# Performance work log

Hardware: AMD Instinct MI355X
Metric: run time of the kernel (lower is better)

Reference implementation:

```python
import jax, jax.numpy as jnp
import numpy as np

B, L, D = 4, 4096, 128
BLOCK, SPARSITY = 64, 0.9
NEG = -1e9


def _make_block_mask(key):
    nb = L // BLOCK
    bm = jax.random.uniform(key, (nb, nb)) > SPARSITY
    bm = bm | jnp.eye(nb, dtype=bool)  # keep diagonal blocks so no row is fully masked
    bm = jnp.tril(bm)
    return jnp.repeat(jnp.repeat(bm, BLOCK, axis=0), BLOCK, axis=1)  # [L, L]


def _xavier(key, shape):
    limit = float(np.sqrt(6.0 / (shape[0] + shape[1])))
    return jax.random.uniform(key, shape, jnp.float32, -limit, limit)


def setup_inputs() -> dict:
    key = jax.random.key(0)
    ks = jax.random.split(key, 10)
    t = lambda k: jax.random.normal(k, (B, L, D), jnp.float32)
    return {
        'q_real': t(ks[0]), 'q_imag': t(ks[1]),
        'k_real': t(ks[2]), 'k_imag': t(ks[3]),
        'v_real': t(ks[4]), 'v_imag': t(ks[5]),
        'W_qkv': _xavier(ks[6], (6 * D, 6 * D)),
        'b_qkv': jnp.zeros((6 * D,), jnp.float32),
        'W_out': _xavier(ks[7], (2 * D, 2 * D)),
        'b_out': jnp.zeros((2 * D,), jnp.float32),
        'block_mask': _make_block_mask(ks[8]),
    }


def reference(q_real, q_imag, k_real, k_imag, v_real, v_imag,
              W_qkv, b_qkv, W_out, b_out, block_mask):
    d = q_real.shape[-1]
    scale = d ** -0.5
    # fused qkv projection over the 6 concatenated channels
    x = jnp.concatenate([q_real, q_imag, k_real, k_imag, v_real, v_imag], axis=-1)  # [B,L,6D]
    qkv = (x @ W_qkv.T + b_qkv).reshape(x.shape[0], x.shape[1], 6, d)
    q_r, q_i, k_r, k_i, v_r, v_i = (qkv[:, :, j] for j in range(6))

    def attn(q, k, v):
        s = jnp.einsum('bqd,bkd->bqk', q, k) * scale          # [B,L,L]
        s = jnp.where(block_mask[None], s, NEG)               # block-sparse mask
        a = jax.nn.softmax(s, axis=-1)                        # dropout = identity (eval)
        return jnp.einsum('bqk,bkd->bqd', a, v)

    out = jnp.concatenate([attn(q_r, k_r, v_r), attn(q_i, k_i, v_i)], axis=-1)  # [B,L,2D]
    out = out @ W_out.T + b_out
    return out[..., :d], out[..., d:]
```

## Files before the change

### kernel.cpp

```cpp
#include <hip/hip_runtime.h>
#include <hip/hip_bf16.h>

typedef unsigned short u16;
typedef __attribute__((ext_vector_type(8))) short bf16x8;
typedef __attribute__((ext_vector_type(4))) float f32x4;

#define SEQ_L 4096
#define M_TOT 16384

__device__ __forceinline__ float bf2f(u16 x) {
    unsigned u = ((unsigned)x) << 16;
    return __builtin_bit_cast(float, u);
}
__device__ __forceinline__ u16 f2bf(float f) {
    unsigned u = __builtin_bit_cast(unsigned, f);
    u += 0x7FFFu + ((u >> 16) & 1u);
    return (u16)(u >> 16);
}
__device__ __forceinline__ void gload16(const u16* g, u16* l) {
    __builtin_amdgcn_global_load_lds(
        (const __attribute__((address_space(1))) unsigned int*)g,
        (__attribute__((address_space(3))) unsigned int*)l, 16, 0, 0);
}

__global__ __launch_bounds__(256) void prep_all(
    const float* __restrict__ in0, const float* __restrict__ in1, const float* __restrict__ in2,
    const float* __restrict__ in3, const float* __restrict__ in4, const float* __restrict__ in5,
    const float* __restrict__ Wqkv, const float* __restrict__ Wout, const void* __restrict__ mask,
    u16* __restrict__ x, u16* __restrict__ Wqkv_bf, u16* __restrict__ Wout_bf,
    unsigned long long* __restrict__ bmap) {
    int id = blockIdx.x * 256 + threadIdx.x;
    if (id < 1572864) {
        const float* ins[6] = {in0, in1, in2, in3, in4, in5};
        int which = id >> 18, j = id & 262143;
        int m = j >> 4, c8 = j & 15;
        const float* sp = ins[which] + (size_t)m * 128 + c8 * 8;
        float4 a = *(const float4*)sp;
        float4 b = *(const float4*)(sp + 4);
        u16 t[8] = {f2bf(a.x), f2bf(a.y), f2bf(a.z), f2bf(a.w),
                    f2bf(b.x), f2bf(b.y), f2bf(b.z), f2bf(b.w)};
        *(uint4*)(x + (size_t)m * 768 + which * 128 + c8 * 8) = *(uint4*)t;
    } else if (id < 1572864 + 73728 + 8192) {
        int i = id - 1572864;
        const float* src = (i < 73728) ? Wqkv : Wout;
        u16* dst = (i < 73728) ? Wqkv_bf : Wout_bf;
        if (i >= 73728) i -= 73728;
        const float* sp = src + (size_t)i * 8;
        float4 a = *(const float4*)sp;
        float4 b = *(const float4*)(sp + 4);
        u16 t[8] = {f2bf(a.x), f2bf(a.y), f2bf(a.z), f2bf(a.w),
                    f2bf(b.x), f2bf(b.y), f2bf(b.z), f2bf(b.w)};
        *(uint4*)(dst + (size_t)i * 8) = *(uint4*)t;
    } else if (id < 1572864 + 73728 + 8192 + 4096) {
        int i = id - 1572864 - 73728 - 8192;
        int bi = i >> 6, bj = i & 63;
        size_t e = (size_t)(bi * 64) * SEQ_L + (size_t)bj * 64;
        const unsigned char* p8 = (const unsigned char*)mask;
        unsigned w0 = *(const unsigned*)mask;
        bool v;
        if (w0 == 0x01010101u || w0 == 0xFFFFFFFFu)      v = p8[e] != 0;
        else if (w0 == 0x3F803F80u || w0 == 0x3C003C00u) v = ((const u16*)mask)[e] != 0;
        else                                             v = ((const unsigned*)mask)[e] != 0;
        unsigned long long bits = __ballot(v);
        if ((i & 63) == 0) bmap[bi] = bits;
    }
}

__global__ __launch_bounds__(256, 3) void qkv_gemm(
    const u16* __restrict__ X, const u16* __restrict__ W, const float* __restrict__ bias,
    u16* __restrict__ qk, u16* __restrict__ vt) {
    __shared__ __align__(16) u16 As[128 * 64];
    __shared__ __align__(16) u16 Bs[128 * 64];
    int m0 = blockIdx.x * 128, n0 = blockIdx.y * 128;
    int tid = threadIdx.x, lane = tid & 63, w = tid >> 6;
    int ln = lane & 15, quad = lane >> 4;
    int rw = (w >> 1) * 64, cw = (w & 1) * 64;
    int lr8 = lane >> 3, lc = lane & 7;
    f32x4 acc[4][4] = {};
    for (int kk = 0; kk < 768; kk += 64) {
        __syncthreads();
        #pragma unroll
        for (int j = 0; j < 4; j++) {
            int r0 = w * 32 + j * 8, r = r0 + lr8;
            gload16(X + (size_t)(m0 + r) * 768 + kk + ((lc ^ (r & 7)) * 8), As + r0 * 64 + lane * 8);
            gload16(W + (size_t)(n0 + r) * 768 + kk + ((lc ^ (r & 7)) * 8), Bs + r0 * 64 + lane * 8);
        }
        __syncthreads();
        #pragma unroll
        for (int s = 0; s < 2; s++) {
            bf16x8 af[4], bfr[4];
            #pragma unroll
            for (int i = 0; i < 4; i++) {
                int R = rw + i * 16 + ln;
                af[i] = *(const bf16x8*)(As + R * 64 + ((4 * s + quad) ^ (ln & 7)) * 8);
            }
            #pragma unroll
            for (int t = 0; t < 4; t++) {
                int R = cw + t * 16 + ln;
                bfr[t] = *(const bf16x8*)(Bs + R * 64 + ((4 * s + quad) ^ (ln & 7)) * 8);
            }
            #pragma unroll
            for (int i = 0; i < 4; i++)
                #pragma unroll
                for (int t = 0; t < 4; t++)
                    acc[i][t] = __builtin_amdgcn_mfma_f32_16x16x32_bf16(af[i], bfr[t], acc[i][t], 0, 0, 0);
        }
    }
    if (n0 < 512) {
        #pragma unroll
        for (int i = 0; i < 4; i++) {
            int row0 = m0 + rw + i * 16 + 4 * quad;
            #pragma unroll
            for (int t = 0; t < 4; t++) {
                int col = n0 + cw + t * 16 + ln;
                float bv = bias[col];
                #pragma unroll
                for (int r = 0; r < 4; r++)
                    qk[(size_t)(row0 + r) * 512 + col] = f2bf(acc[i][t][r] + bv);
            }
        }
    } else {
        #pragma unroll
        for (int i = 0; i < 4; i++) {
            int row0 = m0 + rw + i * 16 + 4 * quad;
            int b = row0 >> 12, seq = row0 & 4095;
            #pragma unroll
            for (int t = 0; t < 4; t++) {
                int col = n0 + cw + t * 16 + ln;
                float bv = bias[col];
                int d = col - 512;
                u16 pk[4] = {f2bf(acc[i][t][0] + bv), f2bf(acc[i][t][1] + bv),
                             f2bf(acc[i][t][2] + bv), f2bf(acc[i][t][3] + bv)};
                *(ushort4*)(vt + ((size_t)(b * 2 + (d >> 7)) * 128 + (d & 127)) * SEQ_L + seq)
                    = *(ushort4*)pk;
            }
        }
    }
}

__global__ __launch_bounds__(256, 2) void attn_sparse(
    const u16* __restrict__ qk, const u16* __restrict__ vt,
    const unsigned long long* __restrict__ bmap, u16* __restrict__ attn_bf) {
    __shared__ __align__(16) u16 Ks[2][64 * 128];
    __shared__ __align__(16) u16 Vs[2][128 * 64];
    __shared__ __align__(16) u16 Psm[4][16 * 72];

    int lane = threadIdx.x & 63, w = threadIdx.x >> 6;
    int ln = lane & 15, quad = lane >> 4;
    int u = blockIdx.x >> 3, v = blockIdx.x & 7;
    int qi = (u < 32) ? (63 - u) : (u - 32);
    int b = v >> 1, ch = v & 1;
    int rowbase = b * SEQ_L + qi * 64 + w * 16;
    const float scale = 0.08838834764831845f;
    u16* Ps = Psm[w];

    bf16x8 qf[4];
    {
        const u16* qp = qk + (size_t)(rowbase + ln) * 512 + ch * 128;
        #pragma unroll
        for (int s = 0; s < 4; s++) qf[s] = *(const bf16x8*)(qp + 32 * s + 8 * quad);
    }
    bf16x8 onesb;
    #pragma unroll
    for (int j = 0; j < 8; j++) onesb[j] = (short)0x3F80;

    float m_st[4];
    #pragma unroll
    for (int r = 0; r < 4; r++) m_st[r] = -1e30f;
    f32x4 accO[8] = {};
    f32x4 accL = {};

    const u16* kbase0 = qk + (size_t)b * SEQ_L * 512 + 256 + ch * 128;
    const u16* vbase0 = vt + (size_t)(b * 2 + ch) * 128 * SEQ_L;
    unsigned long long bm = bmap[qi];

    int kb = __ffsll(bm) - 1; bm &= bm - 1;
    {
        const u16* kp = kbase0 + (size_t)(kb * 64) * 512;
        const u16* vp = vbase0 + kb * 64;
        #pragma unroll
        for (int j = 0; j < 4; j++) {
            int kr = w * 16 + j * 4 + (lane >> 4);
            gload16(kp + (size_t)kr * 512 + (((lane & 15) ^ (kr & 7)) * 8),
                    Ks[0] + (w * 16 + j * 4) * 128 + lane * 8);
        }
        #pragma unroll
        for (int j = 0; j < 4; j++) {
            int d = w * 32 + j * 8 + (lane >> 3);
            gload16(vp + (size_t)d * SEQ_L + (((lane & 7) ^ (d & 7)) * 8),
                    Vs[0] + (w * 32 + j * 8) * 64 + lane * 8);
        }
    }

    int bufc = 0;
    while (true) {
        int nkb = -1;
        if (bm) {
            nkb = __ffsll(bm) - 1; bm &= bm - 1;
            const u16* kp = kbase0 + (size_t)(nkb * 64) * 512;
            const u16* vp = vbase0 + nkb * 64;
            u16* Kd = Ks[bufc ^ 1];
            u16* Vd = Vs[bufc ^ 1];
            #pragma unroll
            for (int j = 0; j < 4; j++) {
                int kr = w * 16 + j * 4 + (lane >> 4);
                gload16(kp + (size_t)kr * 512 + (((lane & 15) ^ (kr & 7)) * 8),
                        Kd + (w * 16 + j * 4) * 128 + lane * 8);
            }
            #pragma unroll
            for (int j = 0; j < 4; j++) {
                int d = w * 32 + j * 8 + (lane >> 3);
                gload16(vp + (size_t)d * SEQ_L + (((lane & 7) ^ (d & 7)) * 8),
                        Vd + (w * 32 + j * 8) * 64 + lane * 8);
            }
        }
        if (nkb >= 0) __builtin_amdgcn_s_waitcnt(0x0F78);
        else          __builtin_amdgcn_s_waitcnt(0x0F70);
        __builtin_amdgcn_s_barrier();

        const u16* K = Ks[bufc];
        const u16* V = Vs[bufc];

        f32x4 accS[4] = {};
        #pragma unroll
        for (int s = 0; s < 4; s++)
            #pragma unroll
            for (int t = 0; t < 4; t++) {
                bf16x8 kf = *(const bf16x8*)(K + (t * 16 + ln) * 128 +
                                             (((4 * s + quad) ^ (ln & 7)) * 8));
                accS[t] = __builtin_amdgcn_mfma_f32_16x16x32_bf16(qf[s], kf, accS[t], 0, 0, 0);
            }

        float mx[4];
        #pragma unroll
        for (int r = 0; r < 4; r++)
            mx[r] = fmaxf(fmaxf(accS[0][r], accS[1][r]),
                          fmaxf(accS[2][r], accS[3][r])) * scale;
        #pragma unroll
        for (int off = 1; off < 16; off <<= 1) {
            float t0 = __shfl_xor(mx[0], off, 64);
            float t1 = __shfl_xor(mx[1], off, 64);
            float t2 = __shfl_xor(mx[2], off, 64);
            float t3 = __shfl_xor(mx[3], off, 64);
            mx[0] = fmaxf(mx[0], t0); mx[1] = fmaxf(mx[1], t1);
            mx[2] = fmaxf(mx[2], t2); mx[3] = fmaxf(mx[3], t3);
        }
        float alpha[4];
        #pragma unroll
        for (int r = 0; r < 4; r++) {
            float nm = fmaxf(m_st[r], mx[r]);
            alpha[r] = __expf(m_st[r] - nm);
            m_st[r] = nm;
        }
        #pragma unroll
        for (int r = 0; r < 4; r++)
            #pragma unroll
            for (int t = 0; t < 4; t++)
                Ps[(4 * quad + r) * 72 + t * 16 + ln] =
                    f2bf(__expf(accS[t][r] * scale - m_st[r]));
        #pragma unroll
        for (int nt = 0; nt < 8; nt++)
            #pragma unroll
            for (int r = 0; r < 4; r++) accO[nt][r] *= alpha[r];
        #pragma unroll
        for (int r = 0; r < 4; r++) accL[r] *= alpha[r];

        #pragma unroll
        for (int h = 0; h < 2; h++) {
            bf16x8 pf = *(const bf16x8*)(Ps + ln * 72 + h * 32 + 8 * quad);
            accL = __builtin_amdgcn_mfma_f32_16x16x32_bf16(pf, onesb, accL, 0, 0, 0);
            #pragma unroll
            for (int nt = 0; nt < 8; nt++) {
                bf16x8 vf = *(const bf16x8*)(V + (nt * 16 + ln) * 64 +
                                             (((4 * h + quad) ^ (ln & 7)) * 8));
                accO[nt] = __builtin_amdgcn_mfma_f32_16x16x32_bf16(pf, vf, accO[nt], 0, 0, 0);
            }
        }

        if (nkb < 0) break;
        __builtin_amdgcn_s_barrier();
        bufc ^= 1;
    }

    float inv[4];
    #pragma unroll
    for (int r = 0; r < 4; r++) inv[r] = 1.0f / fmaxf(accL[r], 1e-20f);
    #pragma unroll
    for (int nt = 0; nt < 8; nt++)
        #pragma unroll
        for (int r = 0; r < 4; r++)
            attn_bf[(size_t)(rowbase + 4 * quad + r) * 256 + ch * 128 + nt * 16 + ln]
                = f2bf(accO[nt][r] * inv[r]);
}

__global__ __launch_bounds__(256) void out_gemm(
    const u16* __restrict__ A, const u16* __restrict__ W, const float* __restrict__ bias,
    float* __restrict__ out) {
    __shared__ __align__(16) u16 As[64 * 64];
    __shared__ __align__(16) u16 Bs[64 * 64];
    int m0 = blockIdx.x * 64, n0 = blockIdx.y * 64;
    int tid = threadIdx.x, lane = tid & 63, w = tid >> 6;
    int ln = lane & 15, quad = lane >> 4;
    int lr8 = lane >> 3, lc = lane & 7;
    int swz_st = lc ^ (lr8 & 7);
    f32x4 acc[4] = {};
    for (int kk = 0; kk < 256; kk += 64) {
        __syncthreads();
        #pragma unroll
        for (int j = 0; j < 2; j++) {
            int r0 = w * 16 + j * 8;
            int r = r0 + lr8;
            gload16(A + (size_t)(m0 + r) * 256 + kk + swz_st * 8, As + r0 * 64 + lane * 8);
            gload16(W + (size_t)(n0 + r) * 256 + kk + swz_st * 8, Bs + r0 * 64 + lane * 8);
        }
        __syncthreads();
        #pragma unroll
        for (int s = 0; s < 2; s++) {
            int R = w * 16 + ln;
            bf16x8 af = *(const bf16x8*)(As + R * 64 + ((4 * s + quad) ^ (ln & 7)) * 8);
            #pragma unroll
            for (int t = 0; t < 4; t++) {
                int Rb = t * 16 + ln;
                bf16x8 bfr = *(const bf16x8*)(Bs + Rb * 64 + ((4 * s + quad) ^ (ln & 7)) * 8);
                acc[t] = __builtin_amdgcn_mfma_f32_16x16x32_bf16(af, bfr, acc[t], 0, 0, 0);
            }
        }
    }
    const size_t half = (size_t)M_TOT * 128;
    #pragma unroll
    for (int t = 0; t < 4; t++) {
        int col = n0 + t * 16 + ln;
        float bv = bias[col];
        float* base = (col < 128) ? (out + col) : (out + half + (col - 128));
        #pragma unroll
        for (int r = 0; r < 4; r++) {
            int row = m0 + w * 16 + 4 * quad + r;
            base[(size_t)row * 128] = acc[t][r] + bv;
        }
    }
}

extern "C" void kernel_launch(void* const* d_in, const int* in_sizes, int n_in,
                              void* d_out, int out_size, void* d_ws, size_t ws_size,
                              hipStream_t stream) {
    char* ws = (char*)d_ws;
    u16* x_bf    = (u16*)ws;
    u16* qk_buf  = x_bf + (size_t)M_TOT * 768;
    u16* vt_buf  = qk_buf + (size_t)M_TOT * 512;
    u16* attn_bf = vt_buf + (size_t)1024 * SEQ_L;
    u16* Wqkv_bf = attn_bf + (size_t)M_TOT * 256;
    u16* Wout_bf = Wqkv_bf + 589824;
    unsigned long long* bmap = (unsigned long long*)(Wout_bf + 65536);

    hipLaunchKernelGGL(prep_all, dim3(6480), dim3(256), 0, stream,
                       (const float*)d_in[0], (const float*)d_in[1], (const float*)d_in[2],
                       (const float*)d_in[3], (const float*)d_in[4], (const float*)d_in[5],
                       (const float*)d_in[6], (const float*)d_in[8], d_in[10],
                       x_bf, Wqkv_bf, Wout_bf, bmap);
    hipLaunchKernelGGL(qkv_gemm, dim3(128, 6), dim3(256), 0, stream,
                       x_bf, Wqkv_bf, (const float*)d_in[7], qk_buf, vt_buf);
    hipLaunchKernelGGL(attn_sparse, dim3(512), dim3(256), 0, stream,
                       qk_buf, vt_buf, bmap, attn_bf);
    hipLaunchKernelGGL(out_gemm, dim3(256, 4), dim3(256), 0, stream,
                       attn_bf, Wout_bf, (const float*)d_in[9], (float*)d_out);
}
```

Before: 195.6 us.

## Compute transposed S tile and pass P to PV MFMA via lane shuffles

Swaps the MFMA operands so each lane holds one query row's scores, which cuts the row max to two cross-lane shuffles and makes the row sum a scalar per lane. The probability tile is packed to bf16 and redistributed into the A-operand layout with register shuffles, so the per-wave LDS staging buffer is gone. The ones-vector MFMA that produced the row sum is also gone. The cost is extra ds_bpermute shuffles and selects, plus broadcasting alpha and the inverse sum back to the output layout.

```diff
diff --git a/kernel.cpp b/kernel.cpp
--- a/kernel.cpp
+++ b/kernel.cpp
@@ -143,7 +143,6 @@
     const unsigned long long* __restrict__ bmap, u16* __restrict__ attn_bf) {
     __shared__ __align__(16) u16 Ks[2][64 * 128];
     __shared__ __align__(16) u16 Vs[2][128 * 64];
-    __shared__ __align__(16) u16 Psm[4][16 * 72];
 
     int lane = threadIdx.x & 63, w = threadIdx.x >> 6;
     int ln = lane & 15, quad = lane >> 4;
@@ -152,7 +151,6 @@
     int b = v >> 1, ch = v & 1;
     int rowbase = b * SEQ_L + qi * 64 + w * 16;
     const float scale = 0.08838834764831845f;
-    u16* Ps = Psm[w];
 
     bf16x8 qf[4];
     {
@@ -160,15 +158,9 @@
         #pragma unroll
         for (int s = 0; s < 4; s++) qf[s] = *(const bf16x8*)(qp + 32 * s + 8 * quad);
     }
-    bf16x8 onesb;
-    #pragma unroll
-    for (int j = 0; j < 8; j++) onesb[j] = (short)0x3F80;
-
-    float m_st[4];
-    #pragma unroll
-    for (int r = 0; r < 4; r++) m_st[r] = -1e30f;
+
+    float m_st = -1e30f, l_st = 0.f;
     f32x4 accO[8] = {};
-    f32x4 accL = {};
 
     const u16* kbase0 = qk + (size_t)b * SEQ_L * 512 + 256 + ch * 128;
     const u16* vbase0 = vt + (size_t)(b * 2 + ch) * 128 * SEQ_L;
@@ -191,6 +183,10 @@
                     Vs[0] + (w * 32 + j * 8) * 64 + lane * 8);
         }
     }
+
+    int srcA = ln + ((quad & 1) << 5);
+    int srcB = srcA + 16;
+    bool hi = (quad & 2) != 0;
 
     int bufc = 0;
     while (true) {
@@ -228,47 +224,63 @@
             for (int t = 0; t < 4; t++) {
                 bf16x8 kf = *(const bf16x8*)(K + (t * 16 + ln) * 128 +
                                              (((4 * s + quad) ^ (ln & 7)) * 8));
-                accS[t] = __builtin_amdgcn_mfma_f32_16x16x32_bf16(qf[s], kf, accS[t], 0, 0, 0);
-            }
-
-        float mx[4];
-        #pragma unroll
-        for (int r = 0; r < 4; r++)
-            mx[r] = fmaxf(fmaxf(accS[0][r], accS[1][r]),
-                          fmaxf(accS[2][r], accS[3][r])) * scale;
-        #pragma unroll
-        for (int off = 1; off < 16; off <<= 1) {
-            float t0 = __shfl_xor(mx[0], off, 64);
-            float t1 = __shfl_xor(mx[1], off, 64);
-            float t2 = __shfl_xor(mx[2], off, 64);
-            float t3 = __shfl_xor(mx[3], off, 64);
-            mx[0] = fmaxf(mx[0], t0); mx[1] = fmaxf(mx[1], t1);
-            mx[2] = fmaxf(mx[2], t2); mx[3] = fmaxf(mx[3], t3);
-        }
-        float alpha[4];
-        #pragma unroll
-        for (int r = 0; r < 4; r++) {
-            float nm = fmaxf(m_st[r], mx[r]);
-            alpha[r] = __expf(m_st[r] - nm);
-            m_st[r] = nm;
-        }
-        #pragma unroll
-        for (int r = 0; r < 4; r++)
-            #pragma unroll
-            for (int t = 0; t < 4; t++)
-                Ps[(4 * quad + r) * 72 + t * 16 + ln] =
-                    f2bf(__expf(accS[t][r] * scale - m_st[r]));
+                accS[t] = __builtin_amdgcn_mfma_f32_16x16x32_bf16(kf, qf[s], accS[t], 0, 0, 0);
+            }
+
+        float mx = fmaxf(fmaxf(fmaxf(accS[0][0], accS[0][1]), fmaxf(accS[0][2], accS[0][3])),
+                         fmaxf(fmaxf(fmaxf(accS[1][0], accS[1][1]), fmaxf(accS[1][2], accS[1][3])),
+                               fmaxf(fmaxf(fmaxf(accS[2][0], accS[2][1]), fmaxf(accS[2][2], accS[2][3])),
+                                     fmaxf(fmaxf(accS[3][0], accS[3][1]), fmaxf(accS[3][2], accS[3][3])))));
+        mx = fmaxf(mx, __shfl_xor(mx, 16, 64));
+        mx = fmaxf(mx, __shfl_xor(mx, 32, 64));
+        float nm = fmaxf(m_st, mx * scale);
+        float alpha = __expf(m_st - nm);
+        m_st = nm;
+
+        float p[4][4];
+        float rs = 0.f;
+        #pragma unroll
+        for (int t = 0; t < 4; t++)
+            #pragma unroll
+            for (int r = 0; r < 4; r++) {
+                p[t][r] = __expf(accS[t][r] * scale - nm);
+                rs += p[t][r];
+            }
+        rs += __shfl_xor(rs, 16, 64);
+        rs += __shfl_xor(rs, 32, 64);
+        l_st = l_st * alpha + rs;
+
+        unsigned uA[4], uB[4];
+        #pragma unroll
+        for (int t = 0; t < 4; t++) {
+            uA[t] = (unsigned)f2bf(p[t][0]) | ((unsigned)f2bf(p[t][1]) << 16);
+            uB[t] = (unsigned)f2bf(p[t][2]) | ((unsigned)f2bf(p[t][3]) << 16);
+        }
+
+        float al[4];
+        #pragma unroll
+        for (int r = 0; r < 4; r++) al[r] = __shfl(alpha, 4 * quad + r, 64);
         #pragma unroll
         for (int nt = 0; nt < 8; nt++)
             #pragma unroll
-            for (int r = 0; r < 4; r++) accO[nt][r] *= alpha[r];
-        #pragma unroll
-        for (int r = 0; r < 4; r++) accL[r] *= alpha[r];
+            for (int r = 0; r < 4; r++) accO[nt][r] *= al[r];
 
         #pragma unroll
         for (int h = 0; h < 2; h++) {
-            bf16x8 pf = *(const bf16x8*)(Ps + ln * 72 + h * 32 + 8 * quad);
-            accL = __builtin_amdgcn_mfma_f32_16x16x32_bf16(pf, onesb, accL, 0, 0, 0);
+            unsigned a0 = (unsigned)__shfl((int)uA[2 * h], srcA, 64);
+            unsigned a1 = (unsigned)__shfl((int)uA[2 * h + 1], srcA, 64);
+            unsigned b0 = (unsigned)__shfl((int)uB[2 * h], srcA, 64);
+            unsigned b1 = (unsigned)__shfl((int)uB[2 * h + 1], srcA, 64);
+            unsigned c0 = (unsigned)__shfl((int)uA[2 * h], srcB, 64);
+            unsigned c1 = (unsigned)__shfl((int)uA[2 * h + 1], srcB, 64);
+            unsigned d0 = (unsigned)__shfl((int)uB[2 * h], srcB, 64);
+            unsigned d1 = (unsigned)__shfl((int)uB[2 * h + 1], srcB, 64);
+            union { unsigned w4[4]; bf16x8 v; } pu;
+            pu.w4[0] = hi ? a1 : a0;
+            pu.w4[1] = hi ? b1 : b0;
+            pu.w4[2] = hi ? c1 : c0;
+            pu.w4[3] = hi ? d1 : d0;
+            bf16x8 pf = pu.v;
             #pragma unroll
             for (int nt = 0; nt < 8; nt++) {
                 bf16x8 vf = *(const bf16x8*)(V + (nt * 16 + ln) * 64 +
@@ -282,9 +294,10 @@
         bufc ^= 1;
     }
 
+    float linv = 1.0f / fmaxf(l_st, 1e-20f);
     float inv[4];
     #pragma unroll
-    for (int r = 0; r < 4; r++) inv[r] = 1.0f / fmaxf(accL[r], 1e-20f);
+    for (int r = 0; r < 4; r++) inv[r] = __shfl(linv, 4 * quad + r, 64);
     #pragma unroll
     for (int nt = 0; nt < 8; nt++)
         #pragma unroll
```

After: 195.3 us. About the same (-0.1%).
